# Kernel tuning notes

Hardware: AMD Instinct MI355X
Metric: run time of the kernel (lower is better)

Reference implementation:

```python
import jax, jax.numpy as jnp
import numpy as np
import math

B, S, D = 1, 2048, 2048
NH, NKV = 32, 8
HD = D // NH  # 64
N_REP = NH // NKV


def _rope_tables(seq_len, head_dim, base=10000.0):
    half = head_dim // 2
    inv_freq = 1.0 / (base ** (np.arange(half, dtype=np.float32) / half))
    ang = np.arange(seq_len, dtype=np.float32)[:, None] * inv_freq[None, :]  # [S, half]
    ang = np.concatenate([ang, ang], axis=-1)  # [S, head_dim]
    cos = jnp.asarray(np.cos(ang))[:, None, :]  # [S, 1, head_dim]
    sin = jnp.asarray(np.sin(ang))[:, None, :]
    return cos, sin


def setup_inputs() -> dict:
    key = jax.random.key(0)
    ks = jax.random.split(key, 5)
    x = jax.random.normal(ks[0], (B, S, D), dtype=jnp.float32)
    cos, sin = _rope_tables(S, HD)
    # causal additive mask, broadcast over batch/heads
    neg = jnp.float32(-1e9)
    causal = jnp.where(jnp.tril(jnp.ones((S, S), dtype=bool)), 0.0, neg)
    mask = causal[None, None, :, :]  # [1,1,S,S]
    scale = 0.02
    wq = jax.random.normal(ks[1], (D, NH * HD), dtype=jnp.float32) * scale
    wk = jax.random.normal(ks[2], (D, NKV * HD), dtype=jnp.float32) * scale
    wv = jax.random.normal(ks[3], (D, NKV * HD), dtype=jnp.float32) * scale
    wo = jax.random.normal(ks[4], (NH * HD, D), dtype=jnp.float32) * scale
    return {"x": x, "cos": cos, "sin": sin, "mask": mask,
            "wq": wq, "wk": wk, "wv": wv, "wo": wo}


def apply_rotary_emb(x, cos, sin):
    # x: [b, s, h, d]; cos/sin: [s, 1, d] (broadcast over b, h)
    half = x.shape[-1] // 2
    x1, x2 = x[..., :half], x[..., half:]
    c, s = cos[..., :half], sin[..., :half]
    return jnp.concatenate([x1 * c - x2 * s, x1 * s + x2 * c], axis=-1)


def reference(x, cos, sin, mask, wq, wk, wv, wo):
    b, s, _ = x.shape
    q = (x @ wq).reshape(b, s, NH, HD)
    k = (x @ wk).reshape(b, s, NKV, HD)
    v = (x @ wv).reshape(b, s, NKV, HD)
    q = apply_rotary_emb(q, cos, sin)
    k = apply_rotary_emb(k, cos, sin)
    new_k, new_v = k, v  # kv cache (no previous cache)
    # GQA: repeat_interleave kv heads to match query heads
    k_rep = jnp.repeat(k, N_REP, axis=2)  # [b, s, NH, HD]
    v_rep = jnp.repeat(v, N_REP, axis=2)
    scores = jnp.einsum('bqhd,bkhd->bhqk', q, k_rep) / math.sqrt(HD)
    scores = scores + mask[:, :, -s:, :]
    attn = jax.nn.softmax(scores.astype(jnp.float32), axis=-1).astype(q.dtype)
    out = jnp.einsum('bhqk,bkhd->bqhd', attn, v_rep).reshape(b, s, NH * HD)
    return out @ wo, new_k, new_v
```

## Files before the change

kernel.cpp:

```cpp
#include <hip/hip_runtime.h>

#define S_LEN 2048
#define NHQ 32
#define NKV 8
#define HD 64
#define DMODEL 2048
#define DKV 512

typedef unsigned short ushort_t;
typedef unsigned int uint_t;

typedef __attribute__((ext_vector_type(8))) short bf16x8;
typedef __attribute__((ext_vector_type(4))) float f32x4;

__device__ __forceinline__ float b2f(ushort_t h) {
  union { uint_t u; float f; } v;
  v.u = ((uint_t)h) << 16;
  return v.f;
}
__device__ __forceinline__ ushort_t f2b(float f) {
  union { float f; uint_t u; } v;
  v.f = f;
  uint_t r = v.u + 0x7fffu + ((v.u >> 16) & 1u);
  return (ushort_t)(r >> 16);
}
__device__ __forceinline__ uint_t pack2(float lo, float hi) {
  return (uint_t)f2b(lo) | ((uint_t)f2b(hi) << 16);
}
__device__ __forceinline__ uint_t cvt_pk_bf16(float lo, float hi) {
  uint_t r;
  asm("v_cvt_pk_bf16_f32 %0, %1, %2" : "=v"(r) : "v"(lo), "v"(hi));
  return r;
}

union BF8 { uint4 v; ushort_t s[8]; };

__device__ __forceinline__ void gl_lds16(const ushort_t* g, ushort_t* l) {
  __builtin_amdgcn_global_load_lds((const __attribute__((address_space(1))) void*)g,
                                   (__attribute__((address_space(3))) void*)l, 16, 0, 0);
}

__global__ void xb_kernel(const float* __restrict__ X, ushort_t* __restrict__ XB) {
  int i = (blockIdx.x * 256 + threadIdx.x) * 8;
  float4 a = *(const float4*)(X + i);
  float4 b = *(const float4*)(X + i + 4);
  BF8 u;
  u.s[0] = f2b(a.x); u.s[1] = f2b(a.y); u.s[2] = f2b(a.z); u.s[3] = f2b(a.w);
  u.s[4] = f2b(b.x); u.s[5] = f2b(b.y); u.s[6] = f2b(b.z); u.s[7] = f2b(b.w);
  *(uint4*)(XB + i) = u.v;
}

__global__ __launch_bounds__(256) void wT_kernel(const float* __restrict__ W,
                                                 ushort_t* __restrict__ WT,
                                                 int K, int N) {
  __shared__ ushort_t T[64][66];
  const int tid = threadIdx.x;
  const int r0 = blockIdx.x * 64;
  const int c0 = blockIdx.y * 64;
  {
    const int rl = tid >> 2, cp = (tid & 3) * 16;
    const float* p = W + (size_t)(r0 + rl) * N + c0 + cp;
    float v[16];
    *(float4*)(v)      = *(const float4*)(p);
    *(float4*)(v + 4)  = *(const float4*)(p + 4);
    *(float4*)(v + 8)  = *(const float4*)(p + 8);
    *(float4*)(v + 12) = *(const float4*)(p + 12);
    #pragma unroll
    for (int j = 0; j < 16; ++j) T[cp + j][rl] = f2b(v[j]);
  }
  __syncthreads();
  {
    const int cl = tid >> 2, rp = (tid & 3) * 16;
    uint_t u[8];
    #pragma unroll
    for (int i = 0; i < 8; ++i) u[i] = *(const uint_t*)&T[cl][rp + 2 * i];
    ushort_t* outp = WT + (size_t)(c0 + cl) * K + r0 + rp;
    *(uint4*)(outp)     = make_uint4(u[0], u[1], u[2], u[3]);
    *(uint4*)(outp + 8) = make_uint4(u[4], u[5], u[6], u[7]);
  }
}

__device__ __forceinline__ void gemm_core_gl(const ushort_t* __restrict__ A,
                                             const ushort_t* __restrict__ BT,
                                             int K, int tile_m, int tile_n,
                                             f32x4 (&acc)[4][2],
                                             ushort_t (*As)[32], ushort_t (*Bs)[32]) {
  const int tid = threadIdx.x;
  const int lane = tid & 63;
  const int w = tid >> 6;
  const int wr = (w >> 1) * 64, wc = (w & 1) * 32;
  const int lm = lane & 15, kq = lane >> 4;

  #pragma unroll
  for (int i = 0; i < 4; ++i)
    #pragma unroll
    for (int j = 0; j < 2; ++j) acc[i][j] = {0.f, 0.f, 0.f, 0.f};

  const ushort_t* ap0 = A  + (size_t)(tile_m + w * 32 + (lane >> 2)) * K + (lane & 3) * 8;
  const ushort_t* ap1 = ap0 + (size_t)16 * K;
  const ushort_t* bp  = BT + (size_t)(tile_n + w * 16 + (lane >> 2)) * K + (lane & 3) * 8;
  ushort_t* asb0 = &As[0][0] + w * 1024;
  ushort_t* asb1 = asb0 + 512;
  ushort_t* bsb  = &Bs[0][0] + w * 512;

  for (int kt = 0; kt < K; kt += 32) {
    __syncthreads();
    gl_lds16(ap0 + kt, asb0);
    gl_lds16(ap1 + kt, asb1);
    gl_lds16(bp  + kt, bsb);
    __syncthreads();
    bf16x8 af[4], bfr[2];
    #pragma unroll
    for (int i = 0; i < 4; ++i) af[i]  = *(const bf16x8*)&As[wr + 16 * i + lm][kq * 8];
    #pragma unroll
    for (int j = 0; j < 2; ++j) bfr[j] = *(const bf16x8*)&Bs[wc + 16 * j + lm][kq * 8];
    #pragma unroll
    for (int i = 0; i < 4; ++i)
      #pragma unroll
      for (int j = 0; j < 2; ++j)
        acc[i][j] = __builtin_amdgcn_mfma_f32_16x16x32_bf16(af[i], bfr[j], acc[i][j], 0, 0, 0);
  }
}

__global__ __launch_bounds__(256) void gemm_proj(const ushort_t* __restrict__ A,
                                                 const ushort_t* __restrict__ BT,
                                                 ushort_t* __restrict__ Qo,
                                                 float* __restrict__ Ko,
                                                 float* __restrict__ Vo) {
  __shared__ ushort_t As[128][32];
  __shared__ ushort_t Bs[64][32];
  const int lane = threadIdx.x & 63;
  const int w = threadIdx.x >> 6;
  const int wr = (w >> 1) * 64, wc = (w & 1) * 32;
  const int lm = lane & 15, kq = lane >> 4;
  const int tile_m = blockIdx.y * 128, tile_n = blockIdx.x * 64;
  f32x4 acc[4][2];
  gemm_core_gl(A, BT, DMODEL, tile_m, tile_n, acc, As, Bs);
  #pragma unroll
  for (int i = 0; i < 4; ++i)
    #pragma unroll
    for (int j = 0; j < 2; ++j)
      #pragma unroll
      for (int r = 0; r < 4; ++r) {
        const int row = tile_m + wr + 16 * i + kq * 4 + r;
        const int col = tile_n + wc + 16 * j + lm;
        const float v = acc[i][j][r];
        if (col < 2048)      Qo[(size_t)row * DMODEL + col] = f2b(v);
        else if (col < 2560) Ko[(size_t)row * DKV + col - 2048] = v;
        else                 Vo[(size_t)row * DKV + col - 2560] = v;
      }
}

__global__ __launch_bounds__(256) void gemm_out(const ushort_t* __restrict__ A,
                                                const ushort_t* __restrict__ BT,
                                                float* __restrict__ C) {
  __shared__ ushort_t As[128][32];
  __shared__ ushort_t Bs[64][32];
  const int lane = threadIdx.x & 63;
  const int w = threadIdx.x >> 6;
  const int wr = (w >> 1) * 64, wc = (w & 1) * 32;
  const int lm = lane & 15, kq = lane >> 4;
  const int tile_m = blockIdx.y * 128, tile_n = blockIdx.x * 64;
  f32x4 acc[4][2];
  gemm_core_gl(A, BT, DMODEL, tile_m, tile_n, acc, As, Bs);
  #pragma unroll
  for (int i = 0; i < 4; ++i)
    #pragma unroll
    for (int j = 0; j < 2; ++j)
      #pragma unroll
      for (int r = 0; r < 4; ++r) {
        const int row = tile_m + wr + 16 * i + kq * 4 + r;
        const int col = tile_n + wc + 16 * j + lm;
        C[(size_t)row * DMODEL + col] = acc[i][j][r];
      }
}

__global__ void rope_kb_kernel(float* Kio, ushort_t* __restrict__ KB,
                               const float* __restrict__ cosT, const float* __restrict__ sinT) {
  int idx = blockIdx.x * 256 + threadIdx.x;
  int d = idx & 31;
  int hk = (idx >> 5) & 7;
  int s = idx >> 8;
  float* p = Kio + (size_t)s * DKV + hk * HD + d;
  float x1 = p[0], x2 = p[32];
  float c = cosT[s * 64 + d], sn = sinT[s * 64 + d];
  float n1 = x1 * c - x2 * sn;
  float n2 = x1 * sn + x2 * c;
  p[0] = n1; p[32] = n2;
  ushort_t* kb = KB + (size_t)hk * S_LEN * HD + (size_t)s * HD + d;
  kb[0] = f2b(n1); kb[32] = f2b(n2);
}

__global__ __launch_bounds__(256) void vt_kernel(const float* __restrict__ V,
                                                 ushort_t* __restrict__ VT) {
  __shared__ ushort_t T[64][66];
  const int tid = threadIdx.x;
  const int s0 = blockIdx.x * 64;
  const int hk = blockIdx.y;
  {
    const int s_l = tid >> 2, dp = (tid & 3) * 16;
    const float* p = V + (size_t)(s0 + s_l) * DKV + hk * HD + dp;
    float v[16];
    *(float4*)(v)      = *(const float4*)(p);
    *(float4*)(v + 4)  = *(const float4*)(p + 4);
    *(float4*)(v + 8)  = *(const float4*)(p + 8);
    *(float4*)(v + 12) = *(const float4*)(p + 12);
    #pragma unroll
    for (int j = 0; j < 16; ++j) T[dp + j][s_l] = f2b(v[j]);
  }
  __syncthreads();
  {
    const int d_l = tid >> 2, sp = (tid & 3) * 16;
    uint_t u[8];
    #pragma unroll
    for (int i = 0; i < 8; ++i) u[i] = *(const uint_t*)&T[d_l][sp + 2 * i];
    ushort_t* outp = VT + (size_t)hk * HD * S_LEN + (size_t)d_l * S_LEN + s0 + sp;
    *(uint4*)(outp)     = make_uint4(u[0], u[1], u[2], u[3]);
    *(uint4*)(outp + 8) = make_uint4(u[4], u[5], u[6], u[7]);
  }
}

__global__ __launch_bounds__(256) void attn_mfma3(const ushort_t* Q,
                                                  const ushort_t* __restrict__ KB,
                                                  const ushort_t* __restrict__ VT,
                                                  const float* __restrict__ cosT,
                                                  const float* __restrict__ sinT,
                                                  ushort_t* O) {
  __shared__ __align__(16) char smem[20480];
  ushort_t (*Ps)[32][66] = (ushort_t (*)[32][66])smem;
  const int wv = threadIdx.x >> 6;
  const int lane = threadIdx.x & 63;
  const int lm = lane & 15, kq = lane >> 4;
  const int h = blockIdx.x >> 5;
  const int pr_ = blockIdx.x & 31;
  const int g = (wv & 2) ? (63 - pr_) : pr_;
  const int half = wv & 1;
  const int q0 = g * 32;
  const int hk = h >> 2;
  const ushort_t* KBh = KB + (size_t)hk * S_LEN * HD;
  const ushort_t* VTh = VT + (size_t)hk * HD * S_LEN;
  const float SCL = 0.125f * 1.44269504f;

  bf16x8 bq[2][2];
  #pragma unroll
  for (int nt = 0; nt < 2; ++nt) {
    const int row = q0 + 16 * nt + lm;
    const ushort_t* qp = Q + (size_t)row * DMODEL + h * HD + 8 * kq;
    bf16x8 x1v = *(const bf16x8*)qp;
    bf16x8 x2v = *(const bf16x8*)(qp + 32);
    const float* cp = cosT + row * 64 + 8 * kq;
    const float* sp = sinT + row * 64 + 8 * kq;
    float c[8], s[8];
    *(float4*)(c)     = *(const float4*)(cp);
    *(float4*)(c + 4) = *(const float4*)(cp + 4);
    *(float4*)(s)     = *(const float4*)(sp);
    *(float4*)(s + 4) = *(const float4*)(sp + 4);
    BF8 o1, o2;
    #pragma unroll
    for (int j = 0; j < 8; ++j) {
      float x1 = b2f((ushort_t)x1v[j]);
      float x2 = b2f((ushort_t)x2v[j]);
      o1.s[j] = f2b((x1 * c[j] - x2 * s[j]) * SCL);
      o2.s[j] = f2b((x1 * s[j] + x2 * c[j]) * SCL);
    }
    bq[nt][0] = *(const bf16x8*)&o1;
    bq[nt][1] = *(const bf16x8*)&o2;
  }

  f32x4 Oa[4][2];
  #pragma unroll
  for (int mt = 0; mt < 4; ++mt) { Oa[mt][0] = {0.f,0.f,0.f,0.f}; Oa[mt][1] = {0.f,0.f,0.f,0.f}; }
  float m[2] = {-1e30f, -1e30f}, l[2] = {0.f, 0.f};

  const int ntiles = (q0 + 31) / 64 + 1;
  for (int t = half; t < ntiles; t += 2) {
    const int base = t * 64;
    f32x4 sc[4][2];
    #pragma unroll
    for (int mt = 0; mt < 4; ++mt) { sc[mt][0] = {0.f,0.f,0.f,0.f}; sc[mt][1] = {0.f,0.f,0.f,0.f}; }
    #pragma unroll
    for (int kc = 0; kc < 2; ++kc) {
      bf16x8 ak[4];
      #pragma unroll
      for (int mt = 0; mt < 4; ++mt)
        ak[mt] = *(const bf16x8*)&KBh[(size_t)(base + 16 * mt + lm) * HD + 8 * kq + 32 * kc];
      __builtin_amdgcn_s_setprio(1);
      #pragma unroll
      for (int mt = 0; mt < 4; ++mt)
        #pragma unroll
        for (int nt = 0; nt < 2; ++nt)
          sc[mt][nt] = __builtin_amdgcn_mfma_f32_16x16x32_bf16(ak[mt], bq[nt][kc], sc[mt][nt], 0, 0, 0);
      __builtin_amdgcn_s_setprio(0);
    }
    const bool diag = (t == ntiles - 1);
    #pragma unroll
    for (int nt = 0; nt < 2; ++nt) {
      const int qg = q0 + 16 * nt + lm;
      if (diag) {
        #pragma unroll
        for (int mt = 0; mt < 4; ++mt)
          #pragma unroll
          for (int r = 0; r < 4; ++r)
            if (base + 16 * mt + 4 * kq + r > qg) sc[mt][nt][r] = -1e9f;
      }
      float mx = sc[0][nt][0];
      #pragma unroll
      for (int mt = 0; mt < 4; ++mt)
        #pragma unroll
        for (int r = 0; r < 4; ++r) mx = fmaxf(mx, sc[mt][nt][r]);
      mx = fmaxf(mx, __shfl_xor(mx, 16));
      mx = fmaxf(mx, __shfl_xor(mx, 32));
      if (!__all(mx <= m[nt] + 8.f)) {
        const float mn = fmaxf(m[nt], mx);
        const float al = exp2f(m[nt] - mn);
        m[nt] = mn;
        l[nt] *= al;
        #pragma unroll
        for (int mt = 0; mt < 4; ++mt)
          #pragma unroll
          for (int r = 0; r < 4; ++r) Oa[mt][nt][r] *= al;
      }
      float sum = 0.f;
      #pragma unroll
      for (int mt = 0; mt < 4; ++mt)
        #pragma unroll
        for (int r = 0; r < 4; ++r) {
          float p = exp2f(sc[mt][nt][r] - m[nt]);
          sc[mt][nt][r] = p;
          sum += p;
        }
      sum += __shfl_xor(sum, 16);
      sum += __shfl_xor(sum, 32);
      l[nt] += sum;
      ushort_t* pw = &Ps[wv][16 * nt + lm][4 * kq];
      #pragma unroll
      for (int mt = 0; mt < 4; ++mt) {
        *(uint_t*)(pw + 16 * mt)     = cvt_pk_bf16(sc[mt][nt][0], sc[mt][nt][1]);
        *(uint_t*)(pw + 16 * mt + 2) = cvt_pk_bf16(sc[mt][nt][2], sc[mt][nt][3]);
      }
    }
    #pragma unroll
    for (int kc = 0; kc < 2; ++kc) {
      bf16x8 av[4], pb[2];
      #pragma unroll
      for (int mt = 0; mt < 4; ++mt)
        av[mt] = *(const bf16x8*)&VTh[(size_t)(16 * mt + lm) * S_LEN + base + 8 * kq + 32 * kc];
      #pragma unroll
      for (int nt = 0; nt < 2; ++nt) {
        const ushort_t* prr = &Ps[wv][16 * nt + lm][8 * kq + 32 * kc];
        union { uint_t u[4]; bf16x8 v; } pu;
        pu.u[0] = *(const uint_t*)(prr);
        pu.u[1] = *(const uint_t*)(prr + 2);
        pu.u[2] = *(const uint_t*)(prr + 4);
        pu.u[3] = *(const uint_t*)(prr + 6);
        pb[nt] = pu.v;
      }
      __builtin_amdgcn_s_setprio(1);
      #pragma unroll
      for (int mt = 0; mt < 4; ++mt)
        #pragma unroll
        for (int nt = 0; nt < 2; ++nt)
          Oa[mt][nt] = __builtin_amdgcn_mfma_f32_16x16x32_bf16(av[mt], pb[nt], Oa[mt][nt], 0, 0, 0);
      __builtin_amdgcn_s_setprio(0);
    }
  }

  __syncthreads();
  float* CoB = (float*)smem;
  float* CmB = (float*)smem + 2 * 64 * 36;
  float* ClB = CmB + 2 * 2 * 64;
  const int pair = wv >> 1;
  if (half) {
    float* myo = CoB + (size_t)(pair * 64 + lane) * 36;
    #pragma unroll
    for (int mt = 0; mt < 4; ++mt)
      #pragma unroll
      for (int nt = 0; nt < 2; ++nt)
        *(f32x4*)(myo + (mt * 2 + nt) * 4) = Oa[mt][nt];
    #pragma unroll
    for (int nt = 0; nt < 2; ++nt) {
      CmB[(pair * 2 + nt) * 64 + lane] = m[nt];
      ClB[(pair * 2 + nt) * 64 + lane] = l[nt];
    }
  }
  __syncthreads();
  if (!half) {
    const float* po = CoB + (size_t)(pair * 64 + lane) * 36;
    #pragma unroll
    for (int nt = 0; nt < 2; ++nt) {
      const float m1 = CmB[(pair * 2 + nt) * 64 + lane];
      const float l1 = ClB[(pair * 2 + nt) * 64 + lane];
      const float mn = fmaxf(m[nt], m1);
      const float a0 = exp2f(m[nt] - mn);
      const float a1 = exp2f(m1 - mn);
      const float inv = 1.f / (l[nt] * a0 + l1 * a1);
      ushort_t* orow = O + (size_t)(q0 + 16 * nt + lm) * DMODEL + h * HD + 4 * kq;
      #pragma unroll
      for (int mt = 0; mt < 4; ++mt) {
        const f32x4 o1 = *(const f32x4*)(po + (mt * 2 + nt) * 4);
        const float v0 = (Oa[mt][nt][0] * a0 + o1[0] * a1) * inv;
        const float v1 = (Oa[mt][nt][1] * a0 + o1[1] * a1) * inv;
        const float v2 = (Oa[mt][nt][2] * a0 + o1[2] * a1) * inv;
        const float v3 = (Oa[mt][nt][3] * a0 + o1[3] * a1) * inv;
        *(uint_t*)(orow + 16 * mt)     = cvt_pk_bf16(v0, v1);
        *(uint_t*)(orow + 16 * mt + 2) = cvt_pk_bf16(v2, v3);
      }
    }
  }
}

extern "C" void kernel_launch(void* const* d_in, const int* in_sizes, int n_in,
                              void* d_out, int out_size, void* d_ws, size_t ws_size,
                              hipStream_t stream) {
  const float* x    = (const float*)d_in[0];
  const float* cosT = (const float*)d_in[1];
  const float* sinT = (const float*)d_in[2];
  const float* wq   = (const float*)d_in[4];
  const float* wk   = (const float*)d_in[5];
  const float* wv   = (const float*)d_in[6];
  const float* wo   = (const float*)d_in[7];

  float* out   = (float*)d_out;
  float* out_k = out + (size_t)S_LEN * DMODEL;
  float* out_v = out_k + (size_t)S_LEN * DKV;

  const size_t MB = 1024 * 1024;
  ushort_t* ws    = (ushort_t*)d_ws;
  ushort_t* wqT   = ws;
  ushort_t* wkT   = ws + 4 * MB;
  ushort_t* ws_q  = ws + 6 * MB;
  ushort_t* ws_kb = ws + 10 * MB;
  ushort_t* ws_vt = ws + 11 * MB;
  ushort_t* xb    = (ushort_t*)out;

  dim3 blk(256);
  xb_kernel<<<(S_LEN * DMODEL / 8) / 256, 256, 0, stream>>>(x, xb);
  wT_kernel<<<dim3(32, 32), blk, 0, stream>>>(wq, wqT, DMODEL, DMODEL);
  wT_kernel<<<dim3(32, 8),  blk, 0, stream>>>(wk, wkT, DMODEL, DKV);
  wT_kernel<<<dim3(32, 8),  blk, 0, stream>>>(wv, wkT + (size_t)DKV * DMODEL, DMODEL, DKV);
  gemm_proj<<<dim3(3072 / 64, S_LEN / 128), blk, 0, stream>>>(xb, wqT, ws_q, out_k, out_v);
  wT_kernel<<<dim3(32, 32), blk, 0, stream>>>(wo, wqT, DMODEL, DMODEL);
  rope_kb_kernel<<<(S_LEN * NKV * 32) / 256, 256, 0, stream>>>(out_k, ws_kb, cosT, sinT);
  vt_kernel<<<dim3(S_LEN / 64, NKV), blk, 0, stream>>>(out_v, ws_vt);
  attn_mfma3<<<NHQ * 32, 256, 0, stream>>>(ws_q, ws_kb, ws_vt, cosT, sinT, ws_q);
  gemm_out<<<dim3(DMODEL / 64, S_LEN / 128), blk, 0, stream>>>(ws_q, wqT, out);
}
```

Baseline: 308.5 us.

## Split each query block's KV tiles across four waves with heaviest-first ordering

The attention kernel now gives each block a single 32-row query tile and splits its KV tiles across all four waves, where before two waves split the tiles of each of two paired tiles. The grid is doubled and ordered so the longest causal rows launch first. Cross-lane sum reductions are deferred until after the loop, the max shuffle runs only when a rescale is needed, P stores and loads are widened to vector accesses with a padded LDS row, and setprio hints are removed. The intent is better load balance and occupancy, at the cost of a larger four-way LDS merge at the end and more blocks.

Result: slower. 350.8 us (+13.7%).

```diff
diff --git a/kernel.cpp b/kernel.cpp
--- a/kernel.cpp
+++ b/kernel.cpp
@@ -23,9 +23,6 @@
   v.f = f;
   uint_t r = v.u + 0x7fffu + ((v.u >> 16) & 1u);
   return (ushort_t)(r >> 16);
-}
-__device__ __forceinline__ uint_t pack2(float lo, float hi) {
-  return (uint_t)f2b(lo) | ((uint_t)f2b(hi) << 16);
 }
 __device__ __forceinline__ uint_t cvt_pk_bf16(float lo, float hi) {
   uint_t r;
@@ -220,21 +217,19 @@
   }
 }
 
-__global__ __launch_bounds__(256) void attn_mfma3(const ushort_t* Q,
-                                                  const ushort_t* __restrict__ KB,
-                                                  const ushort_t* __restrict__ VT,
-                                                  const float* __restrict__ cosT,
-                                                  const float* __restrict__ sinT,
-                                                  ushort_t* O) {
-  __shared__ __align__(16) char smem[20480];
-  ushort_t (*Ps)[32][66] = (ushort_t (*)[32][66])smem;
+__global__ __launch_bounds__(256, 5) void attn_mfma4(const ushort_t* Q,
+                                                     const ushort_t* __restrict__ KB,
+                                                     const ushort_t* __restrict__ VT,
+                                                     const float* __restrict__ cosT,
+                                                     const float* __restrict__ sinT,
+                                                     ushort_t* O) {
+  __shared__ __align__(16) char smem[30720];
+  ushort_t (*Ps)[32][72] = (ushort_t (*)[32][72])smem;
   const int wv = threadIdx.x >> 6;
   const int lane = threadIdx.x & 63;
   const int lm = lane & 15, kq = lane >> 4;
-  const int h = blockIdx.x >> 5;
-  const int pr_ = blockIdx.x & 31;
-  const int g = (wv & 2) ? (63 - pr_) : pr_;
-  const int half = wv & 1;
+  const int h = blockIdx.x & 31;
+  const int g = 63 - (blockIdx.x >> 5);
   const int q0 = g * 32;
   const int hk = h >> 2;
   const ushort_t* KBh = KB + (size_t)hk * S_LEN * HD;
@@ -270,10 +265,11 @@
   f32x4 Oa[4][2];
   #pragma unroll
   for (int mt = 0; mt < 4; ++mt) { Oa[mt][0] = {0.f,0.f,0.f,0.f}; Oa[mt][1] = {0.f,0.f,0.f,0.f}; }
-  float m[2] = {-1e30f, -1e30f}, l[2] = {0.f, 0.f};
-
-  const int ntiles = (q0 + 31) / 64 + 1;
-  for (int t = half; t < ntiles; t += 2) {
+  float m[2] = {-1e30f, -1e30f};
+  float l[2] = {0.f, 0.f};
+
+  const int ntiles = (g >> 1) + 1;
+  for (int t = wv; t < ntiles; t += 4) {
     const int base = t * 64;
     f32x4 sc[4][2];
     #pragma unroll
@@ -284,13 +280,11 @@
       #pragma unroll
       for (int mt = 0; mt < 4; ++mt)
         ak[mt] = *(const bf16x8*)&KBh[(size_t)(base + 16 * mt + lm) * HD + 8 * kq + 32 * kc];
-      __builtin_amdgcn_s_setprio(1);
       #pragma unroll
       for (int mt = 0; mt < 4; ++mt)
         #pragma unroll
         for (int nt = 0; nt < 2; ++nt)
           sc[mt][nt] = __builtin_amdgcn_mfma_f32_16x16x32_bf16(ak[mt], bq[nt][kc], sc[mt][nt], 0, 0, 0);
-      __builtin_amdgcn_s_setprio(0);
     }
     const bool diag = (t == ntiles - 1);
     #pragma unroll
@@ -303,14 +297,14 @@
           for (int r = 0; r < 4; ++r)
             if (base + 16 * mt + 4 * kq + r > qg) sc[mt][nt][r] = -1e9f;
       }
-      float mx = sc[0][nt][0];
-      #pragma unroll
-      for (int mt = 0; mt < 4; ++mt)
-        #pragma unroll
-        for (int r = 0; r < 4; ++r) mx = fmaxf(mx, sc[mt][nt][r]);
-      mx = fmaxf(mx, __shfl_xor(mx, 16));
-      mx = fmaxf(mx, __shfl_xor(mx, 32));
-      if (!__all(mx <= m[nt] + 8.f)) {
+      float lmx = sc[0][nt][0];
+      #pragma unroll
+      for (int mt = 0; mt < 4; ++mt)
+        #pragma unroll
+        for (int r = 0; r < 4; ++r) lmx = fmaxf(lmx, sc[mt][nt][r]);
+      if (!__all(lmx <= m[nt] + 8.f)) {
+        float mx = fmaxf(lmx, __shfl_xor(lmx, 16));
+        mx = fmaxf(mx, __shfl_xor(mx, 32));
         const float mn = fmaxf(m[nt], mx);
         const float al = exp2f(m[nt] - mn);
         m[nt] = mn;
@@ -329,15 +323,12 @@
           sc[mt][nt][r] = p;
           sum += p;
         }
-      sum += __shfl_xor(sum, 16);
-      sum += __shfl_xor(sum, 32);
       l[nt] += sum;
       ushort_t* pw = &Ps[wv][16 * nt + lm][4 * kq];
       #pragma unroll
-      for (int mt = 0; mt < 4; ++mt) {
-        *(uint_t*)(pw + 16 * mt)     = cvt_pk_bf16(sc[mt][nt][0], sc[mt][nt][1]);
-        *(uint_t*)(pw + 16 * mt + 2) = cvt_pk_bf16(sc[mt][nt][2], sc[mt][nt][3]);
-      }
+      for (int mt = 0; mt < 4; ++mt)
+        *(uint2*)(pw + 16 * mt) = make_uint2(cvt_pk_bf16(sc[mt][nt][0], sc[mt][nt][1]),
+                                             cvt_pk_bf16(sc[mt][nt][2], sc[mt][nt][3]));
     }
     #pragma unroll
     for (int kc = 0; kc < 2; ++kc) {
@@ -346,32 +337,27 @@
       for (int mt = 0; mt < 4; ++mt)
         av[mt] = *(const bf16x8*)&VTh[(size_t)(16 * mt + lm) * S_LEN + base + 8 * kq + 32 * kc];
       #pragma unroll
-      for (int nt = 0; nt < 2; ++nt) {
-        const ushort_t* prr = &Ps[wv][16 * nt + lm][8 * kq + 32 * kc];
-        union { uint_t u[4]; bf16x8 v; } pu;
-        pu.u[0] = *(const uint_t*)(prr);
-        pu.u[1] = *(const uint_t*)(prr + 2);
-        pu.u[2] = *(const uint_t*)(prr + 4);
-        pu.u[3] = *(const uint_t*)(prr + 6);
-        pb[nt] = pu.v;
-      }
-      __builtin_amdgcn_s_setprio(1);
+      for (int nt = 0; nt < 2; ++nt)
+        pb[nt] = *(const bf16x8*)&Ps[wv][16 * nt + lm][8 * kq + 32 * kc];
       #pragma unroll
       for (int mt = 0; mt < 4; ++mt)
         #pragma unroll
         for (int nt = 0; nt < 2; ++nt)
           Oa[mt][nt] = __builtin_amdgcn_mfma_f32_16x16x32_bf16(av[mt], pb[nt], Oa[mt][nt], 0, 0, 0);
-      __builtin_amdgcn_s_setprio(0);
-    }
+    }
+  }
+  #pragma unroll
+  for (int nt = 0; nt < 2; ++nt) {
+    l[nt] += __shfl_xor(l[nt], 16);
+    l[nt] += __shfl_xor(l[nt], 32);
   }
 
   __syncthreads();
   float* CoB = (float*)smem;
-  float* CmB = (float*)smem + 2 * 64 * 36;
-  float* ClB = CmB + 2 * 2 * 64;
-  const int pair = wv >> 1;
-  if (half) {
-    float* myo = CoB + (size_t)(pair * 64 + lane) * 36;
+  float* CmB = (float*)smem + 3 * 64 * 36;
+  float* ClB = CmB + 3 * 2 * 64;
+  if (wv) {
+    float* myo = CoB + (size_t)((wv - 1) * 64 + lane) * 36;
     #pragma unroll
     for (int mt = 0; mt < 4; ++mt)
       #pragma unroll
@@ -379,31 +365,41 @@
         *(f32x4*)(myo + (mt * 2 + nt) * 4) = Oa[mt][nt];
     #pragma unroll
     for (int nt = 0; nt < 2; ++nt) {
-      CmB[(pair * 2 + nt) * 64 + lane] = m[nt];
-      ClB[(pair * 2 + nt) * 64 + lane] = l[nt];
+      CmB[((wv - 1) * 2 + nt) * 64 + lane] = m[nt];
+      ClB[((wv - 1) * 2 + nt) * 64 + lane] = l[nt];
     }
   }
   __syncthreads();
-  if (!half) {
-    const float* po = CoB + (size_t)(pair * 64 + lane) * 36;
+  if (wv == 0) {
     #pragma unroll
     for (int nt = 0; nt < 2; ++nt) {
-      const float m1 = CmB[(pair * 2 + nt) * 64 + lane];
-      const float l1 = ClB[(pair * 2 + nt) * 64 + lane];
-      const float mn = fmaxf(m[nt], m1);
+      float mw[3], lw[3];
+      #pragma unroll
+      for (int i = 0; i < 3; ++i) {
+        mw[i] = CmB[(i * 2 + nt) * 64 + lane];
+        lw[i] = ClB[(i * 2 + nt) * 64 + lane];
+      }
+      const float mn = fmaxf(fmaxf(m[nt], mw[0]), fmaxf(mw[1], mw[2]));
       const float a0 = exp2f(m[nt] - mn);
-      const float a1 = exp2f(m1 - mn);
-      const float inv = 1.f / (l[nt] * a0 + l1 * a1);
+      float aw[3];
+      float lt = l[nt] * a0;
+      #pragma unroll
+      for (int i = 0; i < 3; ++i) { aw[i] = exp2f(mw[i] - mn); lt += lw[i] * aw[i]; }
+      const float inv = 1.f / lt;
       ushort_t* orow = O + (size_t)(q0 + 16 * nt + lm) * DMODEL + h * HD + 4 * kq;
       #pragma unroll
       for (int mt = 0; mt < 4; ++mt) {
-        const f32x4 o1 = *(const f32x4*)(po + (mt * 2 + nt) * 4);
-        const float v0 = (Oa[mt][nt][0] * a0 + o1[0] * a1) * inv;
-        const float v1 = (Oa[mt][nt][1] * a0 + o1[1] * a1) * inv;
-        const float v2 = (Oa[mt][nt][2] * a0 + o1[2] * a1) * inv;
-        const float v3 = (Oa[mt][nt][3] * a0 + o1[3] * a1) * inv;
-        *(uint_t*)(orow + 16 * mt)     = cvt_pk_bf16(v0, v1);
-        *(uint_t*)(orow + 16 * mt + 2) = cvt_pk_bf16(v2, v3);
+        f32x4 acc;
+        #pragma unroll
+        for (int r = 0; r < 4; ++r) acc[r] = Oa[mt][nt][r] * a0;
+        #pragma unroll
+        for (int i = 0; i < 3; ++i) {
+          const f32x4 ov = *(const f32x4*)(CoB + (size_t)(i * 64 + lane) * 36 + (mt * 2 + nt) * 4);
+          #pragma unroll
+          for (int r = 0; r < 4; ++r) acc[r] += ov[r] * aw[i];
+        }
+        *(uint2*)(orow + 16 * mt) = make_uint2(cvt_pk_bf16(acc[0] * inv, acc[1] * inv),
+                                               cvt_pk_bf16(acc[2] * inv, acc[3] * inv));
       }
     }
   }
@@ -442,6 +438,6 @@
   wT_kernel<<<dim3(32, 32), blk, 0, stream>>>(wo, wqT, DMODEL, DMODEL);
   rope_kb_kernel<<<(S_LEN * NKV * 32) / 256, 256, 0, stream>>>(out_k, ws_kb, cosT, sinT);
   vt_kernel<<<dim3(S_LEN / 64, NKV), blk, 0, stream>>>(out_v, ws_vt);
-  attn_mfma3<<<NHQ * 32, 256, 0, stream>>>(ws_q, ws_kb, ws_vt, cosT, sinT, ws_q);
+  attn_mfma4<<<NHQ * 64, 256, 0, stream>>>(ws_q, ws_kb, ws_vt, cosT, sinT, ws_q);
   gemm_out<<<dim3(DMODEL / 64, S_LEN / 128), blk, 0, stream>>>(ws_q, wqT, out);
 }
```
